# Kernel optimization log

Hardware: AMD Instinct MI355X
Metric: run time of the kernel (lower is better)

## Reference

```python
import jax, jax.numpy as jnp
import numpy as np

B, L, D, E = 16, 1024, 512, 8
DFF = 4 * D
N_VIEWS, N_BUCKETS = 4, 16


def setup_inputs() -> dict:
    key = jax.random.key(0)
    ks = jax.random.split(key, 9)
    s_in = 1.0 / np.sqrt(D)
    s_hid = 1.0 / np.sqrt(DFF)
    return {
        "x": jax.random.normal(ks[0], (B, L, D), dtype=jnp.float32),
        "view_ids": jax.random.randint(ks[1], (B,), 0, N_VIEWS),
        "visit_ids": jax.random.randint(ks[2], (B,), 0, N_BUCKETS),
        "router_view": jax.random.normal(ks[3], (N_VIEWS, E), dtype=jnp.float32),
        "router_visit": jax.random.normal(ks[4], (N_BUCKETS, E), dtype=jnp.float32),
        "W1": jax.random.uniform(ks[5], (E, D, DFF), jnp.float32, -s_in, s_in),
        "b1": jax.random.uniform(ks[6], (E, DFF), jnp.float32, -s_in, s_in),
        "W2": jax.random.uniform(ks[7], (E, DFF, D), jnp.float32, -s_hid, s_hid),
        "b2": jax.random.uniform(ks[8], (E, D), jnp.float32, -s_hid, s_hid),
    }


def reference(x, view_ids, visit_ids, router_view, router_visit, W1, b1, W2, b2):
    # Router: per-sample logits over experts, (B, E)
    logits = router_view[view_ids] + router_visit[visit_ids]
    top1 = jnp.argmax(logits, axis=-1)  # (B,)

    # Train-mode balance loss: load = mean softmax prob per expert, entropy-style term
    probs = jax.nn.softmax(logits, axis=-1)
    load = probs.mean(axis=0)  # (E,)
    balance_loss = -jnp.sum(load * jnp.log(load))

    # Per-sample expert FFN: gather each sample's expert weights (dense grouped GEMM
    # equivalent of the original masked gather->FFN->scatter loop).
    w1 = W1[top1]                      # (B, D, DFF)
    w2 = W2[top1]                      # (B, DFF, D)
    h = jax.nn.relu(jnp.einsum("bld,bdf->blf", x, w1) + b1[top1][:, None, :])
    out = jnp.einsum("blf,bfd->bld", h, w2) + b2[top1][:, None, :]
    return out, balance_loss
```

## Files before the change

kernel.cpp:

```cpp
#include <hip/hip_runtime.h>
#include <stdint.h>

#define B_SZ 16
#define L_SZ 1024
#define D_SZ 512
#define E_SZ 8
#define DFF_SZ 2048

typedef short bf16x8 __attribute__((ext_vector_type(8)));
typedef float f32x4 __attribute__((ext_vector_type(4)));

__device__ __forceinline__ unsigned short f2bf(float f) {
  unsigned int u = __float_as_uint(f);
  u += 0x7fffu + ((u >> 16) & 1u);
  return (unsigned short)(u >> 16);
}

__device__ __forceinline__ void async_cp16(void* lds, const void* g) {
  __builtin_amdgcn_global_load_lds(
      (const __attribute__((address_space(1))) void*)g,
      (__attribute__((address_space(3))) void*)lds, 16, 0, 0);
}

__global__ void router_kernel(const int* __restrict__ view_ids,
                              const int* __restrict__ visit_ids,
                              const float* __restrict__ rview,
                              const float* __restrict__ rvisit,
                              int* __restrict__ top1,
                              float* __restrict__ loss_out) {
  __shared__ float probs[B_SZ][E_SZ];
  const int t = threadIdx.x;
  if (t < B_SZ) {
    const int vi = view_ids[t];
    const int si = visit_ids[t];
    float lg[E_SZ];
#pragma unroll
    for (int e = 0; e < E_SZ; ++e)
      lg[e] = rview[vi * E_SZ + e] + rvisit[si * E_SZ + e];
    int am = 0;
    float bm = lg[0];
#pragma unroll
    for (int e = 1; e < E_SZ; ++e)
      if (lg[e] > bm) { bm = lg[e]; am = e; }
    top1[t] = am;
    float s = 0.f;
#pragma unroll
    for (int e = 0; e < E_SZ; ++e) {
      const float p = expf(lg[e] - bm);
      probs[t][e] = p;
      s += p;
    }
    const float inv = 1.f / s;
#pragma unroll
    for (int e = 0; e < E_SZ; ++e) probs[t][e] *= inv;
  }
  __syncthreads();
  if (t == 0) {
    float loss = 0.f;
#pragma unroll
    for (int e = 0; e < E_SZ; ++e) {
      float ld = 0.f;
      for (int b = 0; b < B_SZ; ++b) ld += probs[b][e];
      ld *= (1.0f / B_SZ);
      loss -= ld * logf(ld);
    }
    *loss_out = loss;
  }
}

__global__ void cast_x_kernel(const float* __restrict__ x,
                              unsigned short* __restrict__ xb) {
  const int i = blockIdx.x * 256 + threadIdx.x;
  const float4 v = reinterpret_cast<const float4*>(x)[i];
  ushort4 o;
  o.x = f2bf(v.x); o.y = f2bf(v.y); o.z = f2bf(v.z); o.w = f2bf(v.w);
  reinterpret_cast<ushort4*>(xb)[i] = o;
}

__global__ void transpose_cast_kernel(const float* __restrict__ src,
                                      unsigned short* __restrict__ dst,
                                      int K, int N) {
  __shared__ float tile[64][65];
  const int e = blockIdx.z;
  const int n0 = blockIdx.x * 64;
  const int k0 = blockIdx.y * 64;
  const int t = threadIdx.x;
  const int c = t & 63;
  const int r4 = t >> 6;
  const float* s = src + ((size_t)e * K + k0) * N + n0;
#pragma unroll
  for (int it = 0; it < 16; ++it) {
    const int k = it * 4 + r4;
    tile[k][c] = s[(size_t)k * N + c];
  }
  __syncthreads();
  unsigned short* d = dst + ((size_t)e * N + n0) * K + k0;
#pragma unroll
  for (int it = 0; it < 16; ++it) {
    const int n = it * 4 + r4;
    d[(size_t)n * K + c] = f2bf(tile[c][n]);
  }
}

template <bool RELU, bool OUT_BF16>
__global__ __launch_bounds__(256, 2) void gemm_kernel(
    const unsigned short* __restrict__ A,
    const unsigned short* __restrict__ BT,
    const float* __restrict__ bias,
    const int* __restrict__ top1,
    void* __restrict__ Out,
    int M, int N, int K) {
  __shared__ __align__(16) unsigned short sm[2][2][128 * 64];

  const int bz = blockIdx.z;
  const int e = top1[bz];
  const int n0 = blockIdx.x * 128;
  const int m0 = blockIdx.y * 128;

  const int t = threadIdx.x;
  const int lane = t & 63;
  const int wid = t >> 6;
  const int wr = wid >> 1, wc = wid & 1;
  const int lr = lane & 15, lg = lane >> 4;

  const size_t Kb = (size_t)K * 2;
  const int srow = t >> 3;
  const int sgr = (t & 7) ^ (srow & 7);
  const char* aSrc = (const char*)(A + (size_t)bz * M * K + (size_t)m0 * K) +
                     (size_t)srow * Kb + sgr * 16;
  const char* bSrc = (const char*)(BT + (size_t)e * N * K + (size_t)n0 * K) +
                     (size_t)srow * Kb + sgr * 16;

  f32x4 acc[4][4] = {};

  const int nk = K >> 6;

  auto stage = [&](int buf, int kt) {
    char* la = (char*)&sm[buf][0][0];
    char* lb = (char*)&sm[buf][1][0];
    const size_t kofs = (size_t)kt * 128;
#pragma unroll
    for (int c = 0; c < 4; ++c) {
      async_cp16(la + c * 4096 + t * 16, aSrc + kofs + (size_t)c * 32 * Kb);
      async_cp16(lb + c * 4096 + t * 16, bSrc + kofs + (size_t)c * 32 * Kb);
    }
  };

  stage(0, 0);
  __syncthreads();

  for (int kt = 0; kt < nk; ++kt) {
    const int cur = kt & 1;
    if (kt + 1 < nk) stage(cur ^ 1, kt + 1);
    const char* la = (const char*)&sm[cur][0][0];
    const char* lb = (const char*)&sm[cur][1][0];
#pragma unroll
    for (int ks = 0; ks < 2; ++ks) {
      bf16x8 af[4], bg[4];
#pragma unroll
      for (int i = 0; i < 4; ++i) {
        const int row = wr * 64 + i * 16 + lr;
        af[i] = *(const bf16x8*)(la + row * 128 +
                                 (((ks * 4 + lg) ^ (row & 7)) << 4));
      }
#pragma unroll
      for (int j = 0; j < 4; ++j) {
        const int row = wc * 64 + j * 16 + lr;
        bg[j] = *(const bf16x8*)(lb + row * 128 +
                                 (((ks * 4 + lg) ^ (row & 7)) << 4));
      }
#pragma unroll
      for (int i = 0; i < 4; ++i)
#pragma unroll
        for (int j = 0; j < 4; ++j)
          acc[i][j] = __builtin_amdgcn_mfma_f32_16x16x32_bf16(
              af[i], bg[j], acc[i][j], 0, 0, 0);
    }
    __syncthreads();
  }

  const float* bb = bias + (size_t)e * N + n0;
  unsigned short* ho = (unsigned short*)Out;
  float* fo = (float*)Out;
  const size_t obase = (size_t)bz * M * N + (size_t)m0 * N + n0;
#pragma unroll
  for (int j = 0; j < 4; ++j) {
    const int col = wc * 64 + j * 16 + lr;
    const float bv = bb[col];
#pragma unroll
    for (int i = 0; i < 4; ++i) {
      const int row0 = wr * 64 + i * 16 + lg * 4;
#pragma unroll
      for (int r = 0; r < 4; ++r) {
        float v = acc[i][j][r] + bv;
        if (RELU) v = fmaxf(v, 0.0f);
        const size_t o = obase + (size_t)(row0 + r) * N + col;
        if (OUT_BF16) ho[o] = f2bf(v);
        else fo[o] = v;
      }
    }
  }
}

extern "C" void kernel_launch(void* const* d_in, const int* in_sizes, int n_in,
                              void* d_out, int out_size, void* d_ws,
                              size_t ws_size, hipStream_t stream) {
  const float* x = (const float*)d_in[0];
  const int* view_ids = (const int*)d_in[1];
  const int* visit_ids = (const int*)d_in[2];
  const float* rview = (const float*)d_in[3];
  const float* rvisit = (const float*)d_in[4];
  const float* W1 = (const float*)d_in[5];
  const float* b1 = (const float*)d_in[6];
  const float* W2 = (const float*)d_in[7];
  const float* b2 = (const float*)d_in[8];
  float* out = (float*)d_out;

  char* ws = (char*)d_ws;
  int* top1 = (int*)ws;
  unsigned short* x_bf = (unsigned short*)(ws + 256);
  unsigned short* w1t = (unsigned short*)(ws + 256 + 16777216L);
  unsigned short* w2t = (unsigned short*)(ws + 256 + 2 * 16777216L);
  unsigned short* h_bf = (unsigned short*)(ws + 256 + 3 * 16777216L);

  router_kernel<<<1, 64, 0, stream>>>(view_ids, visit_ids, rview, rvisit, top1,
                                      out + (size_t)B_SZ * L_SZ * D_SZ);
  cast_x_kernel<<<8192, 256, 0, stream>>>(x, x_bf);
  transpose_cast_kernel<<<dim3(DFF_SZ / 64, D_SZ / 64, E_SZ), 256, 0, stream>>>(
      W1, w1t, D_SZ, DFF_SZ);
  transpose_cast_kernel<<<dim3(D_SZ / 64, DFF_SZ / 64, E_SZ), 256, 0, stream>>>(
      W2, w2t, DFF_SZ, D_SZ);
  gemm_kernel<true, true>
      <<<dim3(DFF_SZ / 128, L_SZ / 128, B_SZ), 256, 0, stream>>>(
          x_bf, w1t, b1, top1, (void*)h_bf, L_SZ, DFF_SZ, D_SZ);
  gemm_kernel<false, false>
      <<<dim3(D_SZ / 128, L_SZ / 128, B_SZ), 256, 0, stream>>>(
          h_bf, w2t, b2, top1, (void*)out, L_SZ, D_SZ, DFF_SZ);
}
```

Measured before the change: 253.3 us.

## Rewrite expert GEMMs as 8-wave 256-row tiles with quadrant-phased LDS pipelining

Both expert GEMMs now use a new 512-thread kernel. Each block computes a 256-row tile, split into four quadrant phases. LDS loads for later K-steps are issued between phases, using explicit vmcnt waits and raw barriers with setprio around the MFMA bursts. Block IDs are remapped across 8-way groups so nearby workgroups share weight tiles in cache. The aim is to hide global-to-LDS latency and raise data reuse per tile, at the cost of more registers and LDS per block, which may reduce occupancy. The hand-written waitcnt logic is fragile if the load count per stage changes.

```diff
diff --git a/kernel.cpp b/kernel.cpp
--- a/kernel.cpp
+++ b/kernel.cpp
@@ -102,104 +102,152 @@
   }
 }
 
-template <bool RELU, bool OUT_BF16>
-__global__ __launch_bounds__(256, 2) void gemm_kernel(
+template <int BN, int WN2, int NTILES, bool RELU, bool OUT_BF16>
+__global__ __launch_bounds__(512, 2) void gemm8_kernel(
     const unsigned short* __restrict__ A,
     const unsigned short* __restrict__ BT,
     const float* __restrict__ bias,
     const int* __restrict__ top1,
     void* __restrict__ Out,
-    int M, int N, int K) {
-  __shared__ __align__(16) unsigned short sm[2][2][128 * 64];
-
-  const int bz = blockIdx.z;
-  const int e = top1[bz];
-  const int n0 = blockIdx.x * 128;
-  const int m0 = blockIdx.y * 128;
+    int N, int K) {
+  constexpr int HB = BN / 2;
+  constexpr int WM2 = 8 / WN2;
+  constexpr int RPA = 128 / WM2;
+  constexpr int RPB = HB / WN2;
+  constexpr int MF = RPA / 16;
+  constexpr int NF = RPB / 16;
+  constexpr int LB = HB / 64;
+  constexpr int ABUF = 2 * 128 * 64;
+  constexpr int BBUF = 2 * HB * 64;
+  constexpr int BUFSZ = ABUF + BBUF;
+
+  __shared__ __align__(16) unsigned short sm[2 * BUFSZ];
 
   const int t = threadIdx.x;
   const int lane = t & 63;
   const int wid = t >> 6;
-  const int wr = wid >> 1, wc = wid & 1;
+  const int wm2 = wid / WN2;
+  const int wn2 = wid % WN2;
   const int lr = lane & 15, lg = lane >> 4;
+
+  const int nwg = gridDim.x;
+  const int bid = blockIdx.x;
+  const int wg = (bid & 7) * (nwg >> 3) + (bid >> 3);
+  const int mt = wg / NTILES;
+  const int nt = wg % NTILES;
+  const int n0 = nt * BN;
+  const int bz = mt >> 2;
+  const int e = top1[bz];
 
   const size_t Kb = (size_t)K * 2;
   const int srow = t >> 3;
   const int sgr = (t & 7) ^ (srow & 7);
-  const char* aSrc = (const char*)(A + (size_t)bz * M * K + (size_t)m0 * K) +
-                     (size_t)srow * Kb + sgr * 16;
-  const char* bSrc = (const char*)(BT + (size_t)e * N * K + (size_t)n0 * K) +
-                     (size_t)srow * Kb + sgr * 16;
-
-  f32x4 acc[4][4] = {};
-
+  const char* aRow = (const char*)A + ((size_t)mt * 256 + srow) * Kb + sgr * 16;
+  const char* bRow =
+      (const char*)BT + ((size_t)e * N + n0 + srow) * Kb + sgr * 16;
+
+  auto stageA = [&](int buf, int half, int kt) {
+    char* dst = (char*)sm + (size_t)(buf * BUFSZ + half * (128 * 64)) * 2 + t * 16;
+    const char* s = aRow + (size_t)(half * 128) * Kb + (size_t)kt * 128;
+    async_cp16(dst, s);
+    async_cp16(dst + 8192, s + 64 * Kb);
+  };
+  auto stageB = [&](int buf, int half, int kt) {
+    char* dst =
+        (char*)sm + (size_t)(buf * BUFSZ + ABUF + half * (HB * 64)) * 2 + t * 16;
+    const char* s = bRow + (size_t)(half * HB) * Kb + (size_t)kt * 128;
+    async_cp16(dst, s);
+    if constexpr (LB == 2) async_cp16(dst + 8192, s + 64 * Kb);
+  };
+
+  f32x4 acc[2][2][MF][NF] = {};
   const int nk = K >> 6;
 
-  auto stage = [&](int buf, int kt) {
-    char* la = (char*)&sm[buf][0][0];
-    char* lb = (char*)&sm[buf][1][0];
-    const size_t kofs = (size_t)kt * 128;
-#pragma unroll
-    for (int c = 0; c < 4; ++c) {
-      async_cp16(la + c * 4096 + t * 16, aSrc + kofs + (size_t)c * 32 * Kb);
-      async_cp16(lb + c * 4096 + t * 16, bSrc + kofs + (size_t)c * 32 * Kb);
-    }
-  };
-
-  stage(0, 0);
-  __syncthreads();
+  stageA(0, 0, 0); stageB(0, 0, 0); stageA(0, 1, 0); stageB(0, 1, 0);
+  stageA(1, 0, 1); stageB(1, 0, 1);
+  if constexpr (LB == 2) asm volatile("s_waitcnt vmcnt(4)" ::: "memory");
+  else                   asm volatile("s_waitcnt vmcnt(3)" ::: "memory");
+  __builtin_amdgcn_s_barrier();
+  asm volatile("" ::: "memory");
+
+#define PHASE(QM, QN, STAGE_STMT, TAIL_STMT)                                   \
+  {                                                                            \
+    const char* ab =                                                           \
+        (const char*)sm + (size_t)(bi * BUFSZ + (QM) * (128 * 64)) * 2;        \
+    const char* bbp =                                                          \
+        (const char*)sm + (size_t)(bi * BUFSZ + ABUF + (QN) * (HB * 64)) * 2;  \
+    bf16x8 af[MF][2], bg[NF][2];                                               \
+    _Pragma("unroll") for (int mf = 0; mf < MF; ++mf) {                        \
+      const int row = wm2 * RPA + mf * 16 + lr;                                \
+      _Pragma("unroll") for (int ks = 0; ks < 2; ++ks)                         \
+          af[mf][ks] = *(const bf16x8*)(ab + row * 128 +                       \
+                                        (((ks * 4 + lg) ^ (lr & 7)) << 4));    \
+    }                                                                          \
+    _Pragma("unroll") for (int nf = 0; nf < NF; ++nf) {                        \
+      const int row = wn2 * RPB + nf * 16 + lr;                                \
+      _Pragma("unroll") for (int ks = 0; ks < 2; ++ks)                         \
+          bg[nf][ks] = *(const bf16x8*)(bbp + row * 128 +                      \
+                                        (((ks * 4 + lg) ^ (lr & 7)) << 4));    \
+    }                                                                          \
+    STAGE_STMT                                                                 \
+    __builtin_amdgcn_s_barrier();                                              \
+    asm volatile("" ::: "memory");                                             \
+    __builtin_amdgcn_s_setprio(1);                                             \
+    _Pragma("unroll") for (int ks = 0; ks < 2; ++ks)                           \
+        _Pragma("unroll") for (int mf = 0; mf < MF; ++mf)                      \
+            _Pragma("unroll") for (int nf = 0; nf < NF; ++nf)                  \
+                acc[QM][QN][mf][nf] = __builtin_amdgcn_mfma_f32_16x16x32_bf16( \
+                    af[mf][ks], bg[nf][ks], acc[QM][QN][mf][nf], 0, 0, 0);     \
+    __builtin_amdgcn_s_setprio(0);                                             \
+    TAIL_STMT                                                                  \
+    __builtin_amdgcn_s_barrier();                                              \
+    asm volatile("" ::: "memory");                                             \
+  }
 
   for (int kt = 0; kt < nk; ++kt) {
-    const int cur = kt & 1;
-    if (kt + 1 < nk) stage(cur ^ 1, kt + 1);
-    const char* la = (const char*)&sm[cur][0][0];
-    const char* lb = (const char*)&sm[cur][1][0];
-#pragma unroll
-    for (int ks = 0; ks < 2; ++ks) {
-      bf16x8 af[4], bg[4];
-#pragma unroll
-      for (int i = 0; i < 4; ++i) {
-        const int row = wr * 64 + i * 16 + lr;
-        af[i] = *(const bf16x8*)(la + row * 128 +
-                                 (((ks * 4 + lg) ^ (row & 7)) << 4));
-      }
-#pragma unroll
-      for (int j = 0; j < 4; ++j) {
-        const int row = wc * 64 + j * 16 + lr;
-        bg[j] = *(const bf16x8*)(lb + row * 128 +
-                                 (((ks * 4 + lg) ^ (row & 7)) << 4));
-      }
-#pragma unroll
-      for (int i = 0; i < 4; ++i)
-#pragma unroll
-        for (int j = 0; j < 4; ++j)
-          acc[i][j] = __builtin_amdgcn_mfma_f32_16x16x32_bf16(
-              af[i], bg[j], acc[i][j], 0, 0, 0);
-    }
-    __syncthreads();
-  }
-
-  const float* bb = bias + (size_t)e * N + n0;
+    const int bi = kt & 1;
+    PHASE(0, 0, { if (kt + 1 < nk) stageA(bi ^ 1, 1, kt + 1); }, {})
+    PHASE(0, 1, { if (kt + 1 < nk) stageB(bi ^ 1, 1, kt + 1); }, {})
+    PHASE(1, 0, { if (kt + 2 < nk) stageA(bi, 0, kt + 2); }, {})
+    PHASE(1, 1, { if (kt + 2 < nk) stageB(bi, 0, kt + 2); },
+          {
+            if (kt + 2 < nk) {
+              if constexpr (LB == 2)
+                asm volatile("s_waitcnt vmcnt(4)" ::: "memory");
+              else
+                asm volatile("s_waitcnt vmcnt(3)" ::: "memory");
+            } else {
+              asm volatile("s_waitcnt vmcnt(0)" ::: "memory");
+            }
+          })
+  }
+#undef PHASE
+
+  const size_t mrow0 = (size_t)mt * 256;
+  const float* bp = bias + (size_t)e * N + n0;
   unsigned short* ho = (unsigned short*)Out;
   float* fo = (float*)Out;
-  const size_t obase = (size_t)bz * M * N + (size_t)m0 * N + n0;
-#pragma unroll
-  for (int j = 0; j < 4; ++j) {
-    const int col = wc * 64 + j * 16 + lr;
-    const float bv = bb[col];
-#pragma unroll
-    for (int i = 0; i < 4; ++i) {
-      const int row0 = wr * 64 + i * 16 + lg * 4;
-#pragma unroll
-      for (int r = 0; r < 4; ++r) {
-        float v = acc[i][j][r] + bv;
-        if (RELU) v = fmaxf(v, 0.0f);
-        const size_t o = obase + (size_t)(row0 + r) * N + col;
-        if (OUT_BF16) ho[o] = f2bf(v);
-        else fo[o] = v;
-      }
+#pragma unroll
+  for (int qm = 0; qm < 2; ++qm)
+#pragma unroll
+    for (int mf = 0; mf < MF; ++mf) {
+      const int row0 = qm * 128 + wm2 * RPA + mf * 16 + lg * 4;
+#pragma unroll
+      for (int qn = 0; qn < 2; ++qn)
+#pragma unroll
+        for (int nf = 0; nf < NF; ++nf) {
+          const int col = qn * HB + wn2 * RPB + nf * 16 + lr;
+          const float bv = bp[col];
+#pragma unroll
+          for (int r = 0; r < 4; ++r) {
+            float v = acc[qm][qn][mf][nf][r] + bv;
+            if (RELU) v = fmaxf(v, 0.f);
+            const size_t o = (mrow0 + row0 + r) * (size_t)N + n0 + col;
+            if (OUT_BF16) ho[o] = f2bf(v);
+            else fo[o] = v;
+          }
+        }
     }
-  }
 }
 
 extern "C" void kernel_launch(void* const* d_in, const int* in_sizes, int n_in,
@@ -230,10 +278,9 @@
       W1, w1t, D_SZ, DFF_SZ);
   transpose_cast_kernel<<<dim3(D_SZ / 64, DFF_SZ / 64, E_SZ), 256, 0, stream>>>(
       W2, w2t, DFF_SZ, D_SZ);
-  gemm_kernel<true, true>
-      <<<dim3(DFF_SZ / 128, L_SZ / 128, B_SZ), 256, 0, stream>>>(
-          x_bf, w1t, b1, top1, (void*)h_bf, L_SZ, DFF_SZ, D_SZ);
-  gemm_kernel<false, false>
-      <<<dim3(D_SZ / 128, L_SZ / 128, B_SZ), 256, 0, stream>>>(
-          h_bf, w2t, b2, top1, (void*)out, L_SZ, D_SZ, DFF_SZ);
-}
+
+  gemm8_kernel<256, 4, 8, true, true><<<512, 512, 0, stream>>>(
+      x_bf, w1t, b1, top1, (void*)h_bf, DFF_SZ, D_SZ);
+  gemm8_kernel<128, 2, 4, false, false><<<256, 512, 0, stream>>>(
+      h_bf, w2t, b2, top1, (void*)out, D_SZ, DFF_SZ);
+}
```

After: 255.1 us. About the same (+0.7%).
